# Kernel optimization log

Measured on AMD Instinct MI355X. Metric: run time of the kernel, lower is better.

Reference implementation:

```python
import jax, jax.numpy as jnp
import numpy as np

KP_EXTENT = 1.2  # influence radius of each kernel point (init arg KP_extent)
SHADOW_COORD = 1e6  # shadow point coordinate for padding (as in original KPConv)


def setup_inputs() -> dict:
    key = jax.random.key(0)
    k1, k2, k3, k4, k5, k6 = jax.random.split(key, 6)
    N, Ns, H, K, Cin, Cout = 20000, 20000, 40, 15, 128, 128
    q_pts = jax.random.uniform(k1, (N, 3), dtype=jnp.float32)
    s_pts = jax.random.uniform(k2, (Ns, 3), dtype=jnp.float32)
    neighb_inds = jax.random.randint(k3, (N, H), 0, Ns, dtype=jnp.int32)
    x = jax.random.normal(k4, (Ns, Cin), dtype=jnp.float32)
    # kernel point positions inside the sphere (stand-in for load_kernels output)
    kernel_points = jax.random.normal(k5, (K, 3), dtype=jnp.float32) * 0.5
    kernel_points = kernel_points.at[0].set(0.0)  # fixed='center'
    weights = jax.random.normal(k6, (K, Cin, Cout), dtype=jnp.float32) * (1.0 / np.sqrt(Cin))
    return {"q_pts": q_pts, "s_pts": s_pts, "neighb_inds": neighb_inds,
            "x": x, "kernel_points": kernel_points, "weights": weights}


def reference(q_pts, s_pts, neighb_inds, x, kernel_points, weights):
    # Pad support points with a far-away shadow point and features with a zero row,
    # so out-of-range neighbor index Ns contributes nothing (original KPConv trick).
    s_pad = jnp.concatenate([s_pts, jnp.full((1, s_pts.shape[1]), SHADOW_COORD, s_pts.dtype)], axis=0)
    x_pad = jnp.concatenate([x, jnp.zeros((1, x.shape[1]), x.dtype)], axis=0)

    # Gather neighbor coords, center on query points: [N, H, 3]
    neighbors = s_pad[neighb_inds] - q_pts[:, None, :]

    # Squared distance to every kernel point: [N, H, K]
    diff = neighbors[:, :, None, :] - kernel_points[None, None, :, :]
    sq_dist = jnp.sum(diff * diff, axis=-1)

    # Linear influence weights, aggregation_mode='sum': [N, K, H]
    all_weights = jnp.clip(1.0 - jnp.sqrt(sq_dist) / KP_EXTENT, 0.0, None)
    all_weights = jnp.swapaxes(all_weights, 1, 2)

    # Gather neighbor features: [N, H, Cin]
    neighb_x = x_pad[neighb_inds]

    # Influence-weighted aggregation over neighbors: [N, K, Cin]
    weighted = jnp.einsum('nkh,nhc->nkc', all_weights, neighb_x)

    # Per-kernel-point linear maps, summed over kernel points: [N, Cout]
    out = jnp.einsum('nkc,kcd->nd', weighted, weights)
    return out
```

## Files before the change

kernel.cpp:

```cpp
#include <hip/hip_runtime.h>

#define KP   15
#define HN   40
#define CIN  128
#define COUT 128
#define KDIM (KP*CIN)
#define KP_EXT_INV (1.0f/1.2f)
#define GBM  32
#define GBK  128

typedef __bf16 bf16x8 __attribute__((ext_vector_type(8)));
typedef __bf16 bf16x4 __attribute__((ext_vector_type(4)));
typedef float  f32x4  __attribute__((ext_vector_type(4)));

__device__ inline void async_copy16(const void* g, void* lds) {
    __builtin_amdgcn_global_load_lds(
        (const __attribute__((address_space(1))) unsigned int*)g,
        (__attribute__((address_space(3))) unsigned int*)lds, 16, 0, 0);
}
#define LGKM0() __asm__ __volatile__("s_waitcnt lgkmcnt(0)" ::: "memory")
#define VM0()   __asm__ __volatile__("s_waitcnt vmcnt(0)"   ::: "memory")

__global__ __launch_bounds__(256)
void kpconv_prep(const float* __restrict__ x, const float* __restrict__ W,
                 __bf16* __restrict__ xb, __bf16* __restrict__ Wt,
                 int nx_elems, int nxB)
{
    __shared__ float sW[32][133];
    const int b = blockIdx.x;
    const int t = threadIdx.x;

    if (b < nxB) {
        const int e0 = (b*256 + t) * 8;
        if (e0 + 8 <= nx_elems) {
            const float4 f0 = *(const float4*)(x + e0);
            const float4 f1 = *(const float4*)(x + e0 + 4);
            bf16x8 v;
            v[0]=(__bf16)f0.x; v[1]=(__bf16)f0.y; v[2]=(__bf16)f0.z; v[3]=(__bf16)f0.w;
            v[4]=(__bf16)f1.x; v[5]=(__bf16)f1.y; v[6]=(__bf16)f1.z; v[7]=(__bf16)f1.w;
            *(bf16x8*)(xb + e0) = v;
        } else {
            for (int e = e0; e < nx_elems; ++e) xb[e] = (__bf16)x[e];
        }
    } else {
        const int kc0 = (b - nxB) * 32;
        #pragma unroll
        for (int i = 0; i < 4; ++i) {
            const int off = t*4 + i*1024;
            const int r = off >> 7, c = off & 127;
            const float4 f = *(const float4*)(W + (size_t)(kc0 + r)*COUT + c);
            sW[r][c+0]=f.x; sW[r][c+1]=f.y; sW[r][c+2]=f.z; sW[r][c+3]=f.w;
        }
        __syncthreads();
        #pragma unroll
        for (int i = 0; i < 2; ++i) {
            const int id = t + i*256;
            const int d  = id >> 2, ch = id & 3;
            bf16x8 v;
            #pragma unroll
            for (int j = 0; j < 8; ++j) v[j] = (__bf16)sW[ch*8 + j][d];
            *(bf16x8*)(Wt + (size_t)d*KDIM + kc0 + ch*8) = v;
        }
    }
}

union SharedU {
    struct { __bf16 sXt[4][4][128][8];
             float4 s_nd[4][HN]; int s_idx[4][HN]; } a;
    struct { __bf16 sA[GBM*GBK]; __bf16 sB[COUT*GBK]; } b;
};

__global__ __launch_bounds__(256, 3)
void kpconv_main(const float* __restrict__ q_pts,
                 const float* __restrict__ s_pts,
                 const int*   __restrict__ nb,
                 const __bf16* __restrict__ xb,
                 const float* __restrict__ kpts,
                 const __bf16* __restrict__ Wt,
                 __bf16* __restrict__ wsA,
                 float* __restrict__ out, int N, int Ns)
{
    __shared__ SharedU sh;

    const int t  = threadIdx.x;
    const int wv = t >> 6;
    const int l  = t & 63;
    const int m  = l & 15;
    const int q  = l >> 4;
    const int m0 = blockIdx.x * GBM;

    {
        float kx=0.f, ky=0.f, kz=0.f;
        if (m < KP) { kx = kpts[m*3+0]; ky = kpts[m*3+1]; kz = kpts[m*3+2]; }
        const float kk  = kx*kx + ky*ky + kz*kz;
        const float kx2 = -2.f*kx, ky2 = -2.f*ky, kz2 = -2.f*kz;

        for (int pi = 0; pi < 8; ++pi) {
            const int n = m0 + wv*8 + pi;

            if (l < HN) {
                int idx = nb[n*HN + l];
                float dx, dy, dz;
                if (idx >= 0 && idx < Ns) {
                    dx = s_pts[idx*3+0] - q_pts[n*3+0];
                    dy = s_pts[idx*3+1] - q_pts[n*3+1];
                    dz = s_pts[idx*3+2] - q_pts[n*3+2];
                } else { idx = 0; dx = dy = dz = 2.0e6f; }
                sh.a.s_idx[wv][l] = idx;
                sh.a.s_nd[wv][l]  = make_float4(dx, dy, dz, dx*dx+dy*dy+dz*dz);
            }
            LGKM0();

            uint4 g[5][2];
            #pragma unroll
            for (int it = 0; it < 5; ++it) {
                const int h0 = (it < 4) ? (it*8 + 2*q) : (32 + 2*q);
                g[it][0] = *(const uint4*)(xb + (size_t)sh.a.s_idx[wv][h0  ]*CIN + m*8);
                g[it][1] = *(const uint4*)(xb + (size_t)sh.a.s_idx[wv][h0+1]*CIN + m*8);
            }

            bf16x8 wfrag[2];
            #pragma unroll
            for (int ks = 0; ks < 2; ++ks) {
                #pragma unroll
                for (int j = 0; j < 8; ++j) {
                    const int h = ks*32 + q*8 + j;
                    float w = 0.f;
                    if (m < KP && h < HN) {
                        const float4 nd = sh.a.s_nd[wv][h];
                        const float d2 = fmaf(nd.x, kx2,
                                         fmaf(nd.y, ky2,
                                         fmaf(nd.z, kz2, nd.w + kk)));
                        const float d = __builtin_amdgcn_sqrtf(d2);
                        w = fmaxf(fmaf(d, -KP_EXT_INV, 1.0f), 0.f);
                    }
                    wfrag[ks][j] = (__bf16)w;
                }
            }

            f32x4 acc[8];
            #pragma unroll
            for (int nt = 0; nt < 8; ++nt) acc[nt] = (f32x4){0.f,0.f,0.f,0.f};

            #pragma unroll
            for (int ks = 0; ks < 2; ++ks) {
                const int itBeg = ks ? 4 : 0;
                const int itEnd = ks ? 5 : 4;
                #pragma unroll
                for (int it = itBeg; it < itEnd; ++it) {
                    const unsigned av[4] = {g[it][0].x, g[it][0].y, g[it][0].z, g[it][0].w};
                    const unsigned bv[4] = {g[it][1].x, g[it][1].y, g[it][1].z, g[it][1].w};
                    const int hc = ks ? 0 : it;
                    unsigned* plane = (unsigned*)&sh.a.sXt[wv][hc][0][0];
                    #pragma unroll
                    for (int j = 0; j < 8; ++j) {
                        const unsigned v = __builtin_amdgcn_perm(
                            bv[j>>1], av[j>>1], (j&1) ? 0x07060302u : 0x05040100u);
                        const int p = m*8 + (j ^ (m & 7));
                        plane[p*4 + q] = v;
                    }
                }
                LGKM0();
                #pragma unroll
                for (int nt = 0; nt < 8; ++nt) {
                    const int cc = nt*16 + m;
                    const int p  = (cc & ~7) | ((cc & 7) ^ ((cc >> 3) & 7));
                    bf16x8 xf = *(const bf16x8*)&sh.a.sXt[wv][q][p][0];
                    acc[nt] = __builtin_amdgcn_mfma_f32_16x16x32_bf16(
                                  xf, wfrag[ks], acc[nt], 0, 0, 0);
                }
            }

            if (m < KP) {
                #pragma unroll
                for (int nt = 0; nt < 8; ++nt) {
                    bf16x4 v;
                    #pragma unroll
                    for (int r = 0; r < 4; ++r) v[r] = (__bf16)acc[nt][r];
                    *(bf16x4*)(wsA + (size_t)n*KDIM + m*CIN + nt*16 + q*4) = v;
                }
            }
        }
    }

    VM0();
    __syncthreads();

    {
        const int rA = t >> 4;
        const int pA = t & 15;

        f32x4 acc[2][2];
        #pragma unroll
        for (int i = 0; i < 2; ++i)
            #pragma unroll
            for (int j = 0; j < 2; ++j) acc[i][j] = (f32x4){0.f,0.f,0.f,0.f};

        for (int k0 = 0; k0 < KDIM; k0 += GBK) {
            #pragma unroll
            for (int pass = 0; pass < 2; ++pass) {
                const int r  = rA + pass*16;
                const int ch = pA ^ (r & 15);
                async_copy16(wsA + (size_t)(m0 + r)*KDIM + k0 + ch*8,
                             (char*)sh.b.sA + pass*4096 + wv*1024 + l*16);
            }
            #pragma unroll
            for (int pass = 0; pass < 8; ++pass) {
                const int r  = rA + pass*16;
                const int ch = pA ^ (r & 15);
                async_copy16(Wt + (size_t)r*KDIM + k0 + ch*8,
                             (char*)sh.b.sB + pass*4096 + wv*1024 + l*16);
            }
            __syncthreads();

            #pragma unroll
            for (int ks = 0; ks < 4; ++ks) {
                bf16x8 af[2], bfr[2];
                #pragma unroll
                for (int mt = 0; mt < 2; ++mt) {
                    const int row = mt*16 + m;
                    const int p   = (ks*4 + q) ^ (row & 15);
                    af[mt] = *(const bf16x8*)&sh.b.sA[row*GBK + p*8];
                }
                #pragma unroll
                for (int j = 0; j < 2; ++j) {
                    const int row = (wv*2 + j)*16 + m;
                    const int p   = (ks*4 + q) ^ (row & 15);
                    bfr[j] = *(const bf16x8*)&sh.b.sB[row*GBK + p*8];
                }
                #pragma unroll
                for (int mt = 0; mt < 2; ++mt)
                    #pragma unroll
                    for (int j = 0; j < 2; ++j)
                        acc[mt][j] = __builtin_amdgcn_mfma_f32_16x16x32_bf16(
                                         af[mt], bfr[j], acc[mt][j], 0, 0, 0);
            }
            __syncthreads();
        }

        #pragma unroll
        for (int mt = 0; mt < 2; ++mt)
            #pragma unroll
            for (int j = 0; j < 2; ++j)
                #pragma unroll
                for (int r = 0; r < 4; ++r)
                    out[(size_t)(m0 + mt*16 + q*4 + r)*COUT
                        + (wv*2+j)*16 + m] = acc[mt][j][r];
    }
}

#define TM 8
#define WSTR (KP*CIN + 4)

__global__ __launch_bounds__(256, 2)
void kpconv_fused(const float* __restrict__ q_pts,
                  const float* __restrict__ s_pts,
                  const int*   __restrict__ nb,
                  const float* __restrict__ x,
                  const float* __restrict__ kpts,
                  const float* __restrict__ W,
                  float* __restrict__ out,
                  int N, int Ns)
{
    __shared__ float s_kp[KP*3];
    __shared__ float s_nd2[HN*3];
    __shared__ int   s_idx2[HN];
    __shared__ float s_w[KP][HN];
    __shared__ float s_wt[TM*WSTR];

    const int t  = threadIdx.x;
    const int n0 = (int)blockIdx.x * TM;
    if (t < KP*3) s_kp[t] = kpts[t];
    const int c = t & (CIN-1);
    const int g = t >> 7;

    for (int mm = 0; mm < TM; ++mm) {
        const int n = n0 + mm;
        if (t < HN) {
            float dx = 1e6f, dy = 1e6f, dz = 1e6f;
            int idx = 0;
            if (n < N) {
                idx = nb[n*HN + t];
                if (idx >= 0 && idx < Ns) {
                    dx = s_pts[idx*3+0] - q_pts[n*3+0];
                    dy = s_pts[idx*3+1] - q_pts[n*3+1];
                    dz = s_pts[idx*3+2] - q_pts[n*3+2];
                } else idx = 0;
            }
            s_idx2[t] = idx;
            s_nd2[t*3+0] = dx; s_nd2[t*3+1] = dy; s_nd2[t*3+2] = dz;
        }
        __syncthreads();
        for (int task = t; task < KP*HN; task += 256) {
            const int k = task / HN;
            const int h = task - k*HN;
            const float dx = s_nd2[h*3+0] - s_kp[k*3+0];
            const float dy = s_nd2[h*3+1] - s_kp[k*3+1];
            const float dz = s_nd2[h*3+2] - s_kp[k*3+2];
            s_w[k][h] = fmaxf(1.0f - sqrtf(dx*dx+dy*dy+dz*dz)*KP_EXT_INV, 0.0f);
        }
        __syncthreads();
        float facc[8];
        #pragma unroll
        for (int j = 0; j < 8; ++j) facc[j] = 0.0f;
        #pragma unroll 8
        for (int h = 0; h < HN; ++h) {
            const float xv = x[s_idx2[h]*CIN + c];
            #pragma unroll
            for (int j = 0; j < 8; ++j) {
                const int k = g + 2*j;
                if (k < KP) facc[j] += s_w[k][h] * xv;
            }
        }
        #pragma unroll
        for (int j = 0; j < 8; ++j) {
            const int k = g + 2*j;
            if (k < KP) s_wt[mm*WSTR + k*CIN + c] = facc[j];
        }
        __syncthreads();
    }

    const int m3 = t >> 5;
    const int d0 = (t & 31) * 4;
    const float* wm = &s_wt[m3*WSTR];
    float ax = 0.f, ay = 0.f, az = 0.f, aw = 0.f;
    #pragma unroll 4
    for (int kc = 0; kc < KP*CIN; ++kc) {
        const float  wvv = wm[kc];
        const float4 wr = *(const float4*)&W[kc*COUT + d0];
        ax += wvv * wr.x; ay += wvv * wr.y; az += wvv * wr.z; aw += wvv * wr.w;
    }
    const int n = n0 + m3;
    if (n < N) {
        float4 o; o.x = ax; o.y = ay; o.z = az; o.w = aw;
        *(float4*)&out[n*COUT + d0] = o;
    }
}

extern "C" void kernel_launch(void* const* d_in, const int* in_sizes, int n_in,
                              void* d_out, int out_size, void* d_ws, size_t ws_size,
                              hipStream_t stream) {
    const float* q_pts = (const float*)d_in[0];
    const float* s_pts = (const float*)d_in[1];
    const int*   nb    = (const int*)  d_in[2];
    const float* x     = (const float*)d_in[3];
    const float* kpts  = (const float*)d_in[4];
    const float* W     = (const float*)d_in[5];
    float* out = (float*)d_out;

    const int N  = in_sizes[0] / 3;
    const int Ns = in_sizes[1] / 3;
    const int nx = in_sizes[3];

    const size_t needA = (size_t)N * KDIM * sizeof(__bf16);
    const size_t needB = (size_t)COUT * KDIM * sizeof(__bf16);
    const size_t needX = (size_t)nx * sizeof(__bf16);

    if (ws_size >= needA + needB + needX && (N % GBM) == 0 && (nx % 8) == 0
        && (KDIM % GBK) == 0) {
        __bf16* wsA = (__bf16*)d_ws;
        __bf16* wsB = (__bf16*)((char*)d_ws + needA);
        __bf16* wsX = (__bf16*)((char*)d_ws + needA + needB);

        const int nxB = (nx/8 + 255) / 256;
        const int nwB = KDIM / 32;
        hipLaunchKernelGGL(kpconv_prep, dim3(nxB + nwB), dim3(256), 0, stream,
                           x, W, wsX, wsB, nx, nxB);
        hipLaunchKernelGGL(kpconv_main, dim3(N/GBM), dim3(256), 0, stream,
                           q_pts, s_pts, nb, wsX, kpts, wsB, wsA, out, N, Ns);
    } else {
        const int grid = (N + TM - 1) / TM;
        hipLaunchKernelGGL(kpconv_fused, dim3(grid), dim3(256), 0, stream,
                           q_pts, s_pts, nb, x, kpts, W, out, N, Ns);
    }
}
```

Baseline: 143.7 us.

## Double kpconv_main block to 512 threads, splitting points and output tiles across 8 waves

```diff
diff --git a/kernel.cpp b/kernel.cpp
--- a/kernel.cpp
+++ b/kernel.cpp
@@ -65,12 +65,12 @@
 }
 
 union SharedU {
-    struct { __bf16 sXt[4][4][128][8];
-             float4 s_nd[4][HN]; int s_idx[4][HN]; } a;
+    struct { __bf16 sXt[8][4][128][8];
+             float4 s_nd[8][HN]; int s_idx[8][HN]; } a;
     struct { __bf16 sA[GBM*GBK]; __bf16 sB[COUT*GBK]; } b;
 };
 
-__global__ __launch_bounds__(256, 3)
+__global__ __launch_bounds__(512, 4)
 void kpconv_main(const float* __restrict__ q_pts,
                  const float* __restrict__ s_pts,
                  const int*   __restrict__ nb,
@@ -95,8 +95,8 @@
         const float kk  = kx*kx + ky*ky + kz*kz;
         const float kx2 = -2.f*kx, ky2 = -2.f*ky, kz2 = -2.f*kz;
 
-        for (int pi = 0; pi < 8; ++pi) {
-            const int n = m0 + wv*8 + pi;
+        for (int pi = 0; pi < 4; ++pi) {
+            const int n = m0 + wv*4 + pi;
 
             if (l < HN) {
                 int idx = nb[n*HN + l];
@@ -187,53 +187,46 @@
     __syncthreads();
 
     {
-        const int rA = t >> 4;
-        const int pA = t & 15;
-
-        f32x4 acc[2][2];
-        #pragma unroll
-        for (int i = 0; i < 2; ++i)
-            #pragma unroll
-            for (int j = 0; j < 2; ++j) acc[i][j] = (f32x4){0.f,0.f,0.f,0.f};
+        const int rB = t >> 4;
+        const int pB = t & 15;
+
+        f32x4 acc[2];
+        acc[0] = (f32x4){0.f,0.f,0.f,0.f};
+        acc[1] = (f32x4){0.f,0.f,0.f,0.f};
 
         for (int k0 = 0; k0 < KDIM; k0 += GBK) {
-            #pragma unroll
-            for (int pass = 0; pass < 2; ++pass) {
-                const int r  = rA + pass*16;
-                const int ch = pA ^ (r & 15);
-                async_copy16(wsA + (size_t)(m0 + r)*KDIM + k0 + ch*8,
-                             (char*)sh.b.sA + pass*4096 + wv*1024 + l*16);
-            }
-            #pragma unroll
-            for (int pass = 0; pass < 8; ++pass) {
-                const int r  = rA + pass*16;
-                const int ch = pA ^ (r & 15);
+            {
+                const int ch = pB ^ (rB & 15);
+                async_copy16(wsA + (size_t)(m0 + rB)*KDIM + k0 + ch*8,
+                             (char*)sh.b.sA + (size_t)t*16);
+            }
+            #pragma unroll
+            for (int pass = 0; pass < 4; ++pass) {
+                const int r  = rB + pass*32;
+                const int ch = pB ^ (r & 15);
                 async_copy16(Wt + (size_t)r*KDIM + k0 + ch*8,
-                             (char*)sh.b.sB + pass*4096 + wv*1024 + l*16);
+                             (char*)sh.b.sB + pass*8192 + (size_t)t*16);
             }
             __syncthreads();
 
             #pragma unroll
             for (int ks = 0; ks < 4; ++ks) {
-                bf16x8 af[2], bfr[2];
+                bf16x8 af[2], bfr;
                 #pragma unroll
                 for (int mt = 0; mt < 2; ++mt) {
                     const int row = mt*16 + m;
                     const int p   = (ks*4 + q) ^ (row & 15);
                     af[mt] = *(const bf16x8*)&sh.b.sA[row*GBK + p*8];
                 }
-                #pragma unroll
-                for (int j = 0; j < 2; ++j) {
-                    const int row = (wv*2 + j)*16 + m;
+                {
+                    const int row = wv*16 + m;
                     const int p   = (ks*4 + q) ^ (row & 15);
-                    bfr[j] = *(const bf16x8*)&sh.b.sB[row*GBK + p*8];
+                    bfr = *(const bf16x8*)&sh.b.sB[row*GBK + p*8];
                 }
                 #pragma unroll
                 for (int mt = 0; mt < 2; ++mt)
-                    #pragma unroll
-                    for (int j = 0; j < 2; ++j)
-                        acc[mt][j] = __builtin_amdgcn_mfma_f32_16x16x32_bf16(
-                                         af[mt], bfr[j], acc[mt][j], 0, 0, 0);
+                    acc[mt] = __builtin_amdgcn_mfma_f32_16x16x32_bf16(
+                                  af[mt], bfr, acc[mt], 0, 0, 0);
             }
             __syncthreads();
         }
@@ -241,11 +234,9 @@
         #pragma unroll
         for (int mt = 0; mt < 2; ++mt)
             #pragma unroll
-            for (int j = 0; j < 2; ++j)
-                #pragma unroll
-                for (int r = 0; r < 4; ++r)
-                    out[(size_t)(m0 + mt*16 + q*4 + r)*COUT
-                        + (wv*2+j)*16 + m] = acc[mt][j][r];
+            for (int r = 0; r < 4; ++r)
+                out[(size_t)(m0 + mt*16 + q*4 + r)*COUT + wv*16 + m]
+                    = acc[mt][r];
     }
 }
 
@@ -366,7 +357,7 @@
         const int nwB = KDIM / 32;
         hipLaunchKernelGGL(kpconv_prep, dim3(nxB + nwB), dim3(256), 0, stream,
                            x, W, wsX, wsB, nx, nxB);
-        hipLaunchKernelGGL(kpconv_main, dim3(N/GBM), dim3(256), 0, stream,
+        hipLaunchKernelGGL(kpconv_main, dim3(N/GBM), dim3(512), 0, stream,
                            q_pts, s_pts, nb, wsX, kpts, wsB, wsA, out, N, Ns);
     } else {
         const int grid = (N + TM - 1) / TM;
```

Result: slower. 148.5 us (+3.4%).
